# Kernel optimization log

Hardware: AMD Instinct MI355X
Metric: run time of the kernel (lower is better)

The kernel has to match this reference:

```python
import jax, jax.numpy as jnp
import numpy as np

B, S, E = 256, 512, 768          # batch, seq_len, embed_dim (= 2*hidden_dim)
MD = 2 * 384 + 1                 # memory feature dim after location column = 769
HOPS, OUT = 3, 3


def setup_inputs() -> dict:
    key = jax.random.key(0)
    ks = jax.random.split(key, 9)
    memory = jax.random.normal(ks[0], (B, S, E), dtype=jnp.float32)
    aspect = jax.random.normal(ks[1], (B, E), dtype=jnp.float32)
    att_w = jax.random.normal(ks[2], (MD + 2 * E,), dtype=jnp.float32) * 0.02
    att_b = jnp.zeros((1,), dtype=jnp.float32)
    gru_w_ih = jax.random.normal(ks[3], (3 * E, MD), dtype=jnp.float32) * 0.02
    gru_w_hh = jax.random.normal(ks[4], (3 * E, E), dtype=jnp.float32) * 0.02
    gru_b_ih = jnp.zeros((3 * E,), dtype=jnp.float32)
    gru_b_hh = jnp.zeros((3 * E,), dtype=jnp.float32)
    dense_w = jax.random.normal(ks[5], (E, OUT), dtype=jnp.float32) * 0.02
    dense_b = jnp.zeros((OUT,), dtype=jnp.float32)
    memory_len = jax.random.randint(ks[6], (B,), S // 2, S + 1, dtype=jnp.int32)
    left_len = jax.random.randint(ks[7], (B,), 0, 64, dtype=jnp.int32)
    aspect_len = jax.random.randint(ks[8], (B,), 1, 8, dtype=jnp.int32)
    return dict(memory=memory, aspect=aspect, att_w=att_w, att_b=att_b,
                gru_w_ih=gru_w_ih, gru_w_hh=gru_w_hh, gru_b_ih=gru_b_ih,
                gru_b_hh=gru_b_hh, dense_w=dense_w, dense_b=dense_b,
                memory_len=memory_len, left_len=left_len, aspect_len=aspect_len,
                hops=HOPS)


def _locationed_memory(memory, memory_len, left_len, aspect_len):
    # Vectorized form of the nested python loop: per-position location-decay
    # weight and signed-offset column u, only for idx < memory_len.
    dt = memory.dtype
    idx = jnp.arange(memory.shape[1], dtype=jnp.int32)[None, :]   # [1,S]
    start = left_len[:, None]
    alen = aspect_len[:, None]
    mlen = memory_len[:, None]
    before = idx < start
    after_off = idx - start - alen + 1
    u = jnp.where(before, idx - start,
                  jnp.where(idx < start + alen, 0, after_off)).astype(dt)
    l = jnp.where(before, start - idx,
                  jnp.where(idx < start + alen, 0, after_off)).astype(dt)
    valid = idx < mlen
    w = jnp.where(valid, 1.0 - l / mlen.astype(dt), 1.0)
    u = jnp.where(valid, u, 0.0)
    mem = memory * w[:, :, None]
    return jnp.concatenate([mem, u[:, :, None]], axis=-1)        # [B,S,MD]


def _gru_cell(x, h, w_ih, w_hh, b_ih, b_hh):
    gi = x @ w_ih.T + b_ih
    gh = h @ w_hh.T + b_hh
    ir, iz, in_ = jnp.split(gi, 3, axis=-1)
    hr, hz, hn = jnp.split(gh, 3, axis=-1)
    r = jax.nn.sigmoid(ir + hr)
    z = jax.nn.sigmoid(iz + hz)
    n = jnp.tanh(in_ + r * hn)
    return (1.0 - z) * n + z * h


def reference(memory, aspect, att_w, att_b, gru_w_ih, gru_w_hh, gru_b_ih,
              gru_b_hh, dense_w, dense_b, memory_len, left_len, aspect_len,
              hops):
    mem = _locationed_memory(memory, memory_len, left_len, aspect_len)
    # att_linear(cat([mem, et, aspect])) split into three small matvecs
    w_mem = att_w[:MD]
    w_et = att_w[MD:MD + E]
    w_asp = att_w[MD + E:]
    g_static = mem @ w_mem + (aspect @ w_asp)[:, None] + att_b[0]  # [B,S]
    et = jnp.zeros_like(aspect)
    for _ in range(hops):
        g = g_static + (et @ w_et)[:, None]                        # [B,S]
        alpha = jax.nn.softmax(g, axis=1)
        i = jnp.einsum('bs,bsd->bd', alpha, mem)                   # [B,MD]
        et = _gru_cell(i, et, gru_w_ih, gru_w_hh, gru_b_ih, gru_b_hh)
    logits = et @ dense_w + dense_b                                # [B,OUT]
    return logits
```

## Files before the change

kernel.cpp:

```cpp
#include <hip/hip_runtime.h>
#include <math.h>

#define Bn 256
#define Sn 512
#define En 768
#define G3n 2304

typedef __attribute__((ext_vector_type(8))) short short8;
typedef __attribute__((ext_vector_type(4))) float f32x4;

__device__ __forceinline__ float sigmoidf_(float x) { return 1.f / (1.f + __expf(-x)); }
__device__ __forceinline__ float tanhf_(float x) {
  float e = __expf(2.f * x);
  return (e - 1.f) / (e + 1.f);
}

__device__ __forceinline__ unsigned short f2bf(float x) {
  unsigned int u = __builtin_bit_cast(unsigned int, x);
  u += 0x7FFFu + ((u >> 16) & 1u);
  return (unsigned short)(u >> 16);
}
__device__ __forceinline__ float bf2f(unsigned short u) {
  unsigned int x = ((unsigned int)u) << 16;
  return __builtin_bit_cast(float, x);
}

__device__ __forceinline__ void loc_uw(int s, int start, int al, int ml, float& u, float& w) {
  float uu;
  if (s < start)            uu = (float)(s - start);
  else if (s < start + al)  uu = 0.f;
  else                      uu = (float)(s - start - al + 1);
  float l = fabsf(uu);
  if (s < ml) { w = 1.f - l / (float)ml; u = uu; }
  else        { w = 1.f; u = 0.f; }
}

__global__ __launch_bounds__(256) void k_convw(const float* __restrict__ w_ih,
                                               const float* __restrict__ w_hh,
                                               unsigned short* __restrict__ wi_bf,
                                               unsigned short* __restrict__ wh_bf) {
  int t = blockIdx.x * 256 + threadIdx.x;
  int idx = t * 8;
  int r = idx / En, c = idx - r * En;
  const float* src;
  unsigned short* dst;
  if (blockIdx.y == 0) { src = w_ih + (size_t)r * 769 + c; dst = wi_bf + idx; }
  else                 { src = w_hh + (size_t)r * En  + c; dst = wh_bf + idx; }
  unsigned int p[4];
#pragma unroll
  for (int j = 0; j < 4; ++j) {
    unsigned int lo = f2bf(src[2 * j]);
    unsigned int hi = f2bf(src[2 * j + 1]);
    p[j] = lo | (hi << 16);
  }
  *reinterpret_cast<uint4*>(dst) = make_uint4(p[0], p[1], p[2], p[3]);
}

__global__ __launch_bounds__(1024) void k_attn(
    const float* __restrict__ mem, const float* __restrict__ att_w,
    const int* __restrict__ mlen, const int* __restrict__ llen, const int* __restrict__ alen,
    float* __restrict__ pacc, float* __restrict__ pm,
    float* __restrict__ pz, float* __restrict__ piu) {
  __shared__ float accL[16][En];
  __shared__ float mL[16], zL[16], iuL[16];
  int bc = blockIdx.x;
  int b = bc >> 1, half = bc & 1;
  int tid = threadIdx.x, wv = tid >> 6, lane = tid & 63;

  float4 w0 = *reinterpret_cast<const float4*>(att_w + lane * 4);
  float4 w1 = *reinterpret_cast<const float4*>(att_w + 256 + lane * 4);
  float4 w2 = *reinterpret_cast<const float4*>(att_w + 512 + lane * 4);
  float wtail = att_w[En];
  int start = llen[b], al = alen[b], ml = mlen[b];
  int s0row = half * 256 + wv * 16;
  const float* base = mem + ((size_t)b * Sn + s0row) * En;

  float m = -1e30f, z = 0.f, iu = 0.f;
  float4 a0 = {0, 0, 0, 0}, a1 = {0, 0, 0, 0}, a2 = {0, 0, 0, 0};
  float4 v0 = *reinterpret_cast<const float4*>(base + lane * 4);
  float4 v1 = *reinterpret_cast<const float4*>(base + 256 + lane * 4);
  float4 v2 = *reinterpret_cast<const float4*>(base + 512 + lane * 4);

  for (int r = 0; r < 16; ++r) {
    float4 c0 = v0, c1 = v1, c2 = v2;
    if (r < 15) {
      const float* nrow = base + (size_t)(r + 1) * En;
      v0 = *reinterpret_cast<const float4*>(nrow + lane * 4);
      v1 = *reinterpret_cast<const float4*>(nrow + 256 + lane * 4);
      v2 = *reinterpret_cast<const float4*>(nrow + 512 + lane * 4);
    }
    float dot = c0.x * w0.x + c0.y * w0.y + c0.z * w0.z + c0.w * w0.w
              + c1.x * w1.x + c1.y * w1.y + c1.z * w1.z + c1.w * w1.w
              + c2.x * w2.x + c2.y * w2.y + c2.z * w2.z + c2.w * w2.w;
#pragma unroll
    for (int off = 32; off; off >>= 1) dot += __shfl_xor(dot, off);
    int s = s0row + r;
    float u, w;
    loc_uw(s, start, al, ml, u, w);
    float g = w * dot + u * wtail;
    if (g > m) {
      float f = __expf(m - g);
      z *= f; iu *= f;
      a0.x *= f; a0.y *= f; a0.z *= f; a0.w *= f;
      a1.x *= f; a1.y *= f; a1.z *= f; a1.w *= f;
      a2.x *= f; a2.y *= f; a2.z *= f; a2.w *= f;
      m = g;
    }
    float e = __expf(g - m);
    z += e; iu += e * u;
    float sc = e * w;
    a0.x += sc * c0.x; a0.y += sc * c0.y; a0.z += sc * c0.z; a0.w += sc * c0.w;
    a1.x += sc * c1.x; a1.y += sc * c1.y; a1.z += sc * c1.z; a1.w += sc * c1.w;
    a2.x += sc * c2.x; a2.y += sc * c2.y; a2.z += sc * c2.z; a2.w += sc * c2.w;
  }

  *reinterpret_cast<float4*>(&accL[wv][lane * 4])       = a0;
  *reinterpret_cast<float4*>(&accL[wv][256 + lane * 4]) = a1;
  *reinterpret_cast<float4*>(&accL[wv][512 + lane * 4]) = a2;
  if (lane == 0) { mL[wv] = m; zL[wv] = z; iuL[wv] = iu; }
  __syncthreads();

  float M = mL[0];
#pragma unroll
  for (int i = 1; i < 16; ++i) M = fmaxf(M, mL[i]);
  float f[16], Z = 0.f, IU = 0.f;
#pragma unroll
  for (int i = 0; i < 16; ++i) {
    f[i] = __expf(mL[i] - M);
    Z += zL[i] * f[i];
    IU += iuL[i] * f[i];
  }
  if (tid < En) {
    float s = 0.f;
#pragma unroll
    for (int i = 0; i < 16; ++i) s += f[i] * accL[i][tid];
    pacc[(size_t)bc * En + tid] = s;
  }
  if (tid == 0) { pm[bc] = M; pz[bc] = Z; piu[bc] = IU; }
}

__global__ __launch_bounds__(256) void k_comb(
    const float* __restrict__ pacc, const float* __restrict__ pm,
    const float* __restrict__ pz, const float* __restrict__ piu,
    unsigned short* __restrict__ ivec_bf, float* __restrict__ ivtail) {
  int b = blockIdx.x, tid = threadIdx.x;
  float m0 = pm[2 * b], m1 = pm[2 * b + 1];
  float M = fmaxf(m0, m1);
  float f0 = __expf(m0 - M), f1 = __expf(m1 - M);
  float Z = pz[2 * b] * f0 + pz[2 * b + 1] * f1;
  float inv = 1.f / Z;
#pragma unroll
  for (int j = 0; j < 3; ++j) {
    int d = tid + j * 256;
    float s = f0 * pacc[(size_t)(2 * b) * En + d] + f1 * pacc[(size_t)(2 * b + 1) * En + d];
    ivec_bf[(size_t)b * En + d] = f2bf(s * inv);
  }
  if (tid == 0) ivtail[b] = (piu[2 * b] * f0 + piu[2 * b + 1] * f1) * inv;
}

template <int MODE>
__global__ __launch_bounds__(256) void k_fused(
    const unsigned short* __restrict__ Abf, const unsigned short* __restrict__ Wbf,
    const float* __restrict__ ivtail, const float* __restrict__ w_ih,
    const float* __restrict__ b_ih, const float* __restrict__ b_hh,
    float* __restrict__ gi, const unsigned short* __restrict__ et_in_bf,
    unsigned short* __restrict__ et_out_bf) {
  __shared__ unsigned short As[32][72];
  __shared__ unsigned short Bs[3][32][72];
  int e0 = blockIdx.x * 32, m0 = blockIdx.y * 32;
  int tid = threadIdx.x;
  int lane = tid & 63, wv = tid >> 6;
  int wm = wv >> 1, we = wv & 1;
  int l15 = lane & 15, l4 = lane >> 4;

  f32x4 acc[3];
#pragma unroll
  for (int g = 0; g < 3; ++g) { acc[g][0] = 0.f; acc[g][1] = 0.f; acc[g][2] = 0.f; acc[g][3] = 0.f; }

  int arow = tid >> 3, ach = tid & 7;
  for (int k0 = 0; k0 < En; k0 += 64) {
    __syncthreads();
    *reinterpret_cast<uint4*>(&As[arow][ach * 8]) =
        *reinterpret_cast<const uint4*>(Abf + (size_t)(m0 + arow) * En + k0 + ach * 8);
#pragma unroll
    for (int i = 0; i < 3; ++i) {
      int idx = tid + i * 256;
      int row = idx >> 3, ch = idx & 7;
      int g = row >> 5, er = row & 31;
      *reinterpret_cast<uint4*>(&Bs[g][er][ch * 8]) =
          *reinterpret_cast<const uint4*>(Wbf + (size_t)(g * En + e0 + er) * En + k0 + ch * 8);
    }
    __syncthreads();
#pragma unroll
    for (int ks = 0; ks < 2; ++ks) {
      short8 a = *reinterpret_cast<const short8*>(&As[wm * 16 + l15][ks * 32 + l4 * 8]);
#pragma unroll
      for (int g = 0; g < 3; ++g) {
        short8 bfr = *reinterpret_cast<const short8*>(&Bs[g][we * 16 + l15][ks * 32 + l4 * 8]);
        acc[g] = __builtin_amdgcn_mfma_f32_16x16x32_bf16(a, bfr, acc[g], 0, 0, 0);
      }
    }
  }

  int ecol = e0 + we * 16 + l15;
  int mbase = m0 + wm * 16 + l4 * 4;
  float bhr = b_hh[ecol], bhz = b_hh[En + ecol], bhn = b_hh[2 * En + ecol];
  if (MODE == 0) {
    float wn0 = w_ih[(size_t)ecol * 769 + En];
    float wn1 = w_ih[(size_t)(En + ecol) * 769 + En];
    float wn2 = w_ih[(size_t)(2 * En + ecol) * 769 + En];
    float bi0 = b_ih[ecol], bi1 = b_ih[En + ecol], bi2 = b_ih[2 * En + ecol];
#pragma unroll
    for (int j = 0; j < 4; ++j) {
      int m = mbase + j;
      float au = ivtail[m];
      float gr = acc[0][j] + au * wn0 + bi0;
      float gz = acc[1][j] + au * wn1 + bi1;
      float gn = acc[2][j] + au * wn2 + bi2;
      gi[(size_t)m * G3n + ecol]          = gr;
      gi[(size_t)m * G3n + En + ecol]     = gz;
      gi[(size_t)m * G3n + 2 * En + ecol] = gn;
      float r = sigmoidf_(gr + bhr);
      float z = sigmoidf_(gz + bhz);
      float n = tanhf_(gn + r * bhn);
      et_out_bf[(size_t)m * En + ecol] = f2bf((1.f - z) * n);
    }
  } else {
#pragma unroll
    for (int j = 0; j < 4; ++j) {
      int m = mbase + j;
      float rr = sigmoidf_(gi[(size_t)m * G3n + ecol] + acc[0][j] + bhr);
      float zz = sigmoidf_(gi[(size_t)m * G3n + En + ecol] + acc[1][j] + bhz);
      float nn = tanhf_(gi[(size_t)m * G3n + 2 * En + ecol] + rr * (acc[2][j] + bhn));
      float h = bf2f(et_in_bf[(size_t)m * En + ecol]);
      et_out_bf[(size_t)m * En + ecol] = f2bf((1.f - zz) * nn + zz * h);
    }
  }
}

__global__ void k_logits(const unsigned short* __restrict__ et_bf,
                         const float* __restrict__ dw,
                         const float* __restrict__ db, float* __restrict__ out) {
  int gtid = blockIdx.x * blockDim.x + threadIdx.x;
  int wid = gtid >> 6;
  int lane = threadIdx.x & 63;
  if (wid >= Bn) return;
  float s0 = 0.f, s1 = 0.f, s2 = 0.f;
  for (int e = lane; e < En; e += 64) {
    float v = bf2f(et_bf[(size_t)wid * En + e]);
    s0 += v * dw[e * 3 + 0];
    s1 += v * dw[e * 3 + 1];
    s2 += v * dw[e * 3 + 2];
  }
#pragma unroll
  for (int off = 32; off; off >>= 1) {
    s0 += __shfl_xor(s0, off);
    s1 += __shfl_xor(s1, off);
    s2 += __shfl_xor(s2, off);
  }
  if (lane == 0) {
    out[wid * 3 + 0] = s0 + db[0];
    out[wid * 3 + 1] = s1 + db[1];
    out[wid * 3 + 2] = s2 + db[2];
  }
}

extern "C" void kernel_launch(void* const* d_in, const int* in_sizes, int n_in,
                              void* d_out, int out_size, void* d_ws, size_t ws_size,
                              hipStream_t stream) {
  const float* memory   = (const float*)d_in[0];
  const float* att_w    = (const float*)d_in[2];
  const float* gru_w_ih = (const float*)d_in[4];
  const float* gru_w_hh = (const float*)d_in[5];
  const float* gru_b_ih = (const float*)d_in[6];
  const float* gru_b_hh = (const float*)d_in[7];
  const float* dense_w  = (const float*)d_in[8];
  const float* dense_b  = (const float*)d_in[9];
  const int* memory_len = (const int*)d_in[10];
  const int* left_len   = (const int*)d_in[11];
  const int* aspect_len = (const int*)d_in[12];
  float* out = (float*)d_out;

  unsigned short* wi_bf   = (unsigned short*)d_ws;
  unsigned short* wh_bf   = wi_bf + (size_t)G3n * En;
  unsigned short* ivec_bf = wh_bf + (size_t)G3n * En;
  unsigned short* eta_bf  = ivec_bf + (size_t)Bn * En;
  unsigned short* etb_bf  = eta_bf + (size_t)Bn * En;
  unsigned short* etc_bf  = etb_bf + (size_t)Bn * En;
  float* ivtail = (float*)(etc_bf + (size_t)Bn * En);
  float* pm     = ivtail + Bn;
  float* pz     = pm + 2 * Bn;
  float* piu    = pz + 2 * Bn;
  float* pacc   = piu + 2 * Bn;
  float* gi     = pacc + (size_t)2 * Bn * En;

  k_convw<<<dim3(G3n * En / 8 / 256, 2), 256, 0, stream>>>(gru_w_ih, gru_w_hh, wi_bf, wh_bf);
  k_attn<<<dim3(2 * Bn), 1024, 0, stream>>>(memory, att_w, memory_len, left_len, aspect_len,
                                            pacc, pm, pz, piu);
  k_comb<<<dim3(Bn), 256, 0, stream>>>(pacc, pm, pz, piu, ivec_bf, ivtail);
  k_fused<0><<<dim3(En / 32, Bn / 32), 256, 0, stream>>>(
      ivec_bf, wi_bf, ivtail, gru_w_ih, gru_b_ih, gru_b_hh, gi, nullptr, eta_bf);
  k_fused<1><<<dim3(En / 32, Bn / 32), 256, 0, stream>>>(
      eta_bf, wh_bf, nullptr, nullptr, nullptr, gru_b_hh, gi, eta_bf, etb_bf);
  k_fused<1><<<dim3(En / 32, Bn / 32), 256, 0, stream>>>(
      etb_bf, wh_bf, nullptr, nullptr, nullptr, gru_b_hh, gi, etb_bf, etc_bf);
  k_logits<<<dim3(Bn / 4), 256, 0, stream>>>(etc_bf, dense_w, dense_b, out);
}
```

Measured before the change: 126.2 us.

## Merge weight conversion into attention kernel and run GRU hops cooperatively

Result: slower. 202.7 us (+60.6%).

```diff
diff --git a/kernel.cpp b/kernel.cpp
--- a/kernel.cpp
+++ b/kernel.cpp
@@ -1,10 +1,14 @@
 #include <hip/hip_runtime.h>
+#include <hip/hip_cooperative_groups.h>
 #include <math.h>
+
+namespace cg = cooperative_groups;
 
 #define Bn 256
 #define Sn 512
 #define En 768
 #define G3n 2304
+#define COOP_BLOCKS 192
 
 typedef __attribute__((ext_vector_type(8))) short short8;
 typedef __attribute__((ext_vector_type(4))) float f32x4;
@@ -35,37 +39,41 @@
   else        { w = 1.f; u = 0.f; }
 }
 
-__global__ __launch_bounds__(256) void k_convw(const float* __restrict__ w_ih,
-                                               const float* __restrict__ w_hh,
-                                               unsigned short* __restrict__ wi_bf,
-                                               unsigned short* __restrict__ wh_bf) {
-  int t = blockIdx.x * 256 + threadIdx.x;
-  int idx = t * 8;
-  int r = idx / En, c = idx - r * En;
-  const float* src;
-  unsigned short* dst;
-  if (blockIdx.y == 0) { src = w_ih + (size_t)r * 769 + c; dst = wi_bf + idx; }
-  else                 { src = w_hh + (size_t)r * En  + c; dst = wh_bf + idx; }
-  unsigned int p[4];
-#pragma unroll
-  for (int j = 0; j < 4; ++j) {
-    unsigned int lo = f2bf(src[2 * j]);
-    unsigned int hi = f2bf(src[2 * j + 1]);
-    p[j] = lo | (hi << 16);
-  }
-  *reinterpret_cast<uint4*>(dst) = make_uint4(p[0], p[1], p[2], p[3]);
-}
-
-__global__ __launch_bounds__(1024) void k_attn(
+__global__ __launch_bounds__(1024) void k_mega(
     const float* __restrict__ mem, const float* __restrict__ att_w,
     const int* __restrict__ mlen, const int* __restrict__ llen, const int* __restrict__ alen,
+    const float* __restrict__ w_ih, const float* __restrict__ w_hh,
     float* __restrict__ pacc, float* __restrict__ pm,
-    float* __restrict__ pz, float* __restrict__ piu) {
+    float* __restrict__ pz, float* __restrict__ piu,
+    unsigned short* __restrict__ wi_bf, unsigned short* __restrict__ wh_bf) {
   __shared__ float accL[16][En];
   __shared__ float mL[16], zL[16], iuL[16];
   int bc = blockIdx.x;
+  int tid = threadIdx.x;
+
+  if (bc >= 512) {
+    int cb = bc - 512;
+    int mat = cb >= 216;
+    int t = (cb - mat * 216) * 1024 + tid;
+    int idx = t * 8;
+    int r = idx / En, c = idx - r * En;
+    const float* src;
+    unsigned short* dst;
+    if (mat == 0) { src = w_ih + (size_t)r * 769 + c; dst = wi_bf + idx; }
+    else          { src = w_hh + (size_t)r * En  + c; dst = wh_bf + idx; }
+    unsigned int p[4];
+#pragma unroll
+    for (int j = 0; j < 4; ++j) {
+      unsigned int lo = f2bf(src[2 * j]);
+      unsigned int hi = f2bf(src[2 * j + 1]);
+      p[j] = lo | (hi << 16);
+    }
+    *reinterpret_cast<uint4*>(dst) = make_uint4(p[0], p[1], p[2], p[3]);
+    return;
+  }
+
   int b = bc >> 1, half = bc & 1;
-  int tid = threadIdx.x, wv = tid >> 6, lane = tid & 63;
+  int wv = tid >> 6, lane = tid & 63;
 
   float4 w0 = *reinterpret_cast<const float4*>(att_w + lane * 4);
   float4 w1 = *reinterpret_cast<const float4*>(att_w + 256 + lane * 4);
@@ -139,129 +147,140 @@
   if (tid == 0) { pm[bc] = M; pz[bc] = Z; piu[bc] = IU; }
 }
 
-__global__ __launch_bounds__(256) void k_comb(
+__global__ __launch_bounds__(256) void k_coop(
     const float* __restrict__ pacc, const float* __restrict__ pm,
     const float* __restrict__ pz, const float* __restrict__ piu,
-    unsigned short* __restrict__ ivec_bf, float* __restrict__ ivtail) {
-  int b = blockIdx.x, tid = threadIdx.x;
-  float m0 = pm[2 * b], m1 = pm[2 * b + 1];
-  float M = fmaxf(m0, m1);
-  float f0 = __expf(m0 - M), f1 = __expf(m1 - M);
-  float Z = pz[2 * b] * f0 + pz[2 * b + 1] * f1;
-  float inv = 1.f / Z;
-#pragma unroll
-  for (int j = 0; j < 3; ++j) {
-    int d = tid + j * 256;
-    float s = f0 * pacc[(size_t)(2 * b) * En + d] + f1 * pacc[(size_t)(2 * b + 1) * En + d];
-    ivec_bf[(size_t)b * En + d] = f2bf(s * inv);
-  }
-  if (tid == 0) ivtail[b] = (piu[2 * b] * f0 + piu[2 * b + 1] * f1) * inv;
-}
-
-template <int MODE>
-__global__ __launch_bounds__(256) void k_fused(
-    const unsigned short* __restrict__ Abf, const unsigned short* __restrict__ Wbf,
-    const float* __restrict__ ivtail, const float* __restrict__ w_ih,
-    const float* __restrict__ b_ih, const float* __restrict__ b_hh,
-    float* __restrict__ gi, const unsigned short* __restrict__ et_in_bf,
-    unsigned short* __restrict__ et_out_bf) {
+    unsigned short* __restrict__ ivec_bf, float* __restrict__ ivtail,
+    const unsigned short* __restrict__ wi_bf, const unsigned short* __restrict__ wh_bf,
+    const float* __restrict__ w_ih, const float* __restrict__ b_ih,
+    const float* __restrict__ b_hh, float* __restrict__ gi,
+    unsigned short* __restrict__ eta_bf, unsigned short* __restrict__ etb_bf,
+    unsigned short* __restrict__ etc_bf,
+    const float* __restrict__ dw, const float* __restrict__ db,
+    float* __restrict__ out) {
+  cg::grid_group grid = cg::this_grid();
   __shared__ unsigned short As[32][72];
   __shared__ unsigned short Bs[3][32][72];
-  int e0 = blockIdx.x * 32, m0 = blockIdx.y * 32;
-  int tid = threadIdx.x;
-  int lane = tid & 63, wv = tid >> 6;
-  int wm = wv >> 1, we = wv & 1;
+  int bid = blockIdx.x, tid = threadIdx.x;
+
+#pragma unroll
+  for (int it = 0; it < 4; ++it) {
+    int flat = (bid * 256 + tid) + it * (COOP_BLOCKS * 256);
+    int b = flat / En, d = flat - b * En;
+    float m0 = pm[2 * b], m1 = pm[2 * b + 1];
+    float M = fmaxf(m0, m1);
+    float f0 = __expf(m0 - M), f1 = __expf(m1 - M);
+    float inv = 1.f / (pz[2 * b] * f0 + pz[2 * b + 1] * f1);
+    float s = f0 * pacc[(size_t)(2 * b) * En + d] + f1 * pacc[(size_t)(2 * b + 1) * En + d];
+    ivec_bf[flat] = f2bf(s * inv);
+  }
+  if (bid == 0) {
+    int b = tid;
+    float m0 = pm[2 * b], m1 = pm[2 * b + 1];
+    float M = fmaxf(m0, m1);
+    float f0 = __expf(m0 - M), f1 = __expf(m1 - M);
+    float inv = 1.f / (pz[2 * b] * f0 + pz[2 * b + 1] * f1);
+    ivtail[b] = (piu[2 * b] * f0 + piu[2 * b + 1] * f1) * inv;
+  }
+  grid.sync();
+
+  int e0 = (bid % 24) * 32, m0t = (bid / 24) * 32;
+  int lane = tid & 63, wvi = tid >> 6;
+  int wm = wvi >> 1, we = wvi & 1;
   int l15 = lane & 15, l4 = lane >> 4;
-
-  f32x4 acc[3];
-#pragma unroll
-  for (int g = 0; g < 3; ++g) { acc[g][0] = 0.f; acc[g][1] = 0.f; acc[g][2] = 0.f; acc[g][3] = 0.f; }
-
   int arow = tid >> 3, ach = tid & 7;
-  for (int k0 = 0; k0 < En; k0 += 64) {
-    __syncthreads();
-    *reinterpret_cast<uint4*>(&As[arow][ach * 8]) =
-        *reinterpret_cast<const uint4*>(Abf + (size_t)(m0 + arow) * En + k0 + ach * 8);
-#pragma unroll
-    for (int i = 0; i < 3; ++i) {
-      int idx = tid + i * 256;
-      int row = idx >> 3, ch = idx & 7;
-      int g = row >> 5, er = row & 31;
-      *reinterpret_cast<uint4*>(&Bs[g][er][ch * 8]) =
-          *reinterpret_cast<const uint4*>(Wbf + (size_t)(g * En + e0 + er) * En + k0 + ch * 8);
-    }
-    __syncthreads();
-#pragma unroll
-    for (int ks = 0; ks < 2; ++ks) {
-      short8 a = *reinterpret_cast<const short8*>(&As[wm * 16 + l15][ks * 32 + l4 * 8]);
-#pragma unroll
-      for (int g = 0; g < 3; ++g) {
-        short8 bfr = *reinterpret_cast<const short8*>(&Bs[g][we * 16 + l15][ks * 32 + l4 * 8]);
-        acc[g] = __builtin_amdgcn_mfma_f32_16x16x32_bf16(a, bfr, acc[g], 0, 0, 0);
+
+  for (int hop = 0; hop < 3; ++hop) {
+    const unsigned short* Abf = (hop == 0) ? ivec_bf : ((hop == 1) ? eta_bf : etb_bf);
+    const unsigned short* Wbf = (hop == 0) ? wi_bf : wh_bf;
+    unsigned short* Obf = (hop == 0) ? eta_bf : ((hop == 1) ? etb_bf : etc_bf);
+
+    f32x4 acc[3];
+#pragma unroll
+    for (int g = 0; g < 3; ++g) { acc[g][0] = 0.f; acc[g][1] = 0.f; acc[g][2] = 0.f; acc[g][3] = 0.f; }
+
+    for (int k0 = 0; k0 < En; k0 += 64) {
+      __syncthreads();
+      *reinterpret_cast<uint4*>(&As[arow][ach * 8]) =
+          *reinterpret_cast<const uint4*>(Abf + (size_t)(m0t + arow) * En + k0 + ach * 8);
+#pragma unroll
+      for (int i = 0; i < 3; ++i) {
+        int idx = tid + i * 256;
+        int row = idx >> 3, ch = idx & 7;
+        int g = row >> 5, er = row & 31;
+        *reinterpret_cast<uint4*>(&Bs[g][er][ch * 8]) =
+            *reinterpret_cast<const uint4*>(Wbf + (size_t)(g * En + e0 + er) * En + k0 + ch * 8);
       }
-    }
-  }
-
-  int ecol = e0 + we * 16 + l15;
-  int mbase = m0 + wm * 16 + l4 * 4;
-  float bhr = b_hh[ecol], bhz = b_hh[En + ecol], bhn = b_hh[2 * En + ecol];
-  if (MODE == 0) {
-    float wn0 = w_ih[(size_t)ecol * 769 + En];
-    float wn1 = w_ih[(size_t)(En + ecol) * 769 + En];
-    float wn2 = w_ih[(size_t)(2 * En + ecol) * 769 + En];
-    float bi0 = b_ih[ecol], bi1 = b_ih[En + ecol], bi2 = b_ih[2 * En + ecol];
-#pragma unroll
-    for (int j = 0; j < 4; ++j) {
-      int m = mbase + j;
-      float au = ivtail[m];
-      float gr = acc[0][j] + au * wn0 + bi0;
-      float gz = acc[1][j] + au * wn1 + bi1;
-      float gn = acc[2][j] + au * wn2 + bi2;
-      gi[(size_t)m * G3n + ecol]          = gr;
-      gi[(size_t)m * G3n + En + ecol]     = gz;
-      gi[(size_t)m * G3n + 2 * En + ecol] = gn;
-      float r = sigmoidf_(gr + bhr);
-      float z = sigmoidf_(gz + bhz);
-      float n = tanhf_(gn + r * bhn);
-      et_out_bf[(size_t)m * En + ecol] = f2bf((1.f - z) * n);
-    }
-  } else {
-#pragma unroll
-    for (int j = 0; j < 4; ++j) {
-      int m = mbase + j;
-      float rr = sigmoidf_(gi[(size_t)m * G3n + ecol] + acc[0][j] + bhr);
-      float zz = sigmoidf_(gi[(size_t)m * G3n + En + ecol] + acc[1][j] + bhz);
-      float nn = tanhf_(gi[(size_t)m * G3n + 2 * En + ecol] + rr * (acc[2][j] + bhn));
-      float h = bf2f(et_in_bf[(size_t)m * En + ecol]);
-      et_out_bf[(size_t)m * En + ecol] = f2bf((1.f - zz) * nn + zz * h);
-    }
-  }
-}
-
-__global__ void k_logits(const unsigned short* __restrict__ et_bf,
-                         const float* __restrict__ dw,
-                         const float* __restrict__ db, float* __restrict__ out) {
-  int gtid = blockIdx.x * blockDim.x + threadIdx.x;
-  int wid = gtid >> 6;
-  int lane = threadIdx.x & 63;
-  if (wid >= Bn) return;
-  float s0 = 0.f, s1 = 0.f, s2 = 0.f;
-  for (int e = lane; e < En; e += 64) {
-    float v = bf2f(et_bf[(size_t)wid * En + e]);
-    s0 += v * dw[e * 3 + 0];
-    s1 += v * dw[e * 3 + 1];
-    s2 += v * dw[e * 3 + 2];
-  }
-#pragma unroll
-  for (int off = 32; off; off >>= 1) {
-    s0 += __shfl_xor(s0, off);
-    s1 += __shfl_xor(s1, off);
-    s2 += __shfl_xor(s2, off);
-  }
-  if (lane == 0) {
-    out[wid * 3 + 0] = s0 + db[0];
-    out[wid * 3 + 1] = s1 + db[1];
-    out[wid * 3 + 2] = s2 + db[2];
+      __syncthreads();
+#pragma unroll
+      for (int ks = 0; ks < 2; ++ks) {
+        short8 a = *reinterpret_cast<const short8*>(&As[wm * 16 + l15][ks * 32 + l4 * 8]);
+#pragma unroll
+        for (int g = 0; g < 3; ++g) {
+          short8 bfr = *reinterpret_cast<const short8*>(&Bs[g][we * 16 + l15][ks * 32 + l4 * 8]);
+          acc[g] = __builtin_amdgcn_mfma_f32_16x16x32_bf16(a, bfr, acc[g], 0, 0, 0);
+        }
+      }
+    }
+
+    int ecol = e0 + we * 16 + l15;
+    int mbase = m0t + wm * 16 + l4 * 4;
+    float bhr = b_hh[ecol], bhz = b_hh[En + ecol], bhn = b_hh[2 * En + ecol];
+    if (hop == 0) {
+      float wn0 = w_ih[(size_t)ecol * 769 + En];
+      float wn1 = w_ih[(size_t)(En + ecol) * 769 + En];
+      float wn2 = w_ih[(size_t)(2 * En + ecol) * 769 + En];
+      float bi0 = b_ih[ecol], bi1 = b_ih[En + ecol], bi2 = b_ih[2 * En + ecol];
+#pragma unroll
+      for (int j = 0; j < 4; ++j) {
+        int m = mbase + j;
+        float au = ivtail[m];
+        float gr = acc[0][j] + au * wn0 + bi0;
+        float gz = acc[1][j] + au * wn1 + bi1;
+        float gn = acc[2][j] + au * wn2 + bi2;
+        gi[(size_t)m * G3n + ecol]          = gr;
+        gi[(size_t)m * G3n + En + ecol]     = gz;
+        gi[(size_t)m * G3n + 2 * En + ecol] = gn;
+        float r = sigmoidf_(gr + bhr);
+        float z = sigmoidf_(gz + bhz);
+        float n = tanhf_(gn + r * bhn);
+        Obf[(size_t)m * En + ecol] = f2bf((1.f - z) * n);
+      }
+    } else {
+#pragma unroll
+      for (int j = 0; j < 4; ++j) {
+        int m = mbase + j;
+        float rr = sigmoidf_(gi[(size_t)m * G3n + ecol] + acc[0][j] + bhr);
+        float zz = sigmoidf_(gi[(size_t)m * G3n + En + ecol] + acc[1][j] + bhz);
+        float nn = tanhf_(gi[(size_t)m * G3n + 2 * En + ecol] + rr * (acc[2][j] + bhn));
+        float h = bf2f(Abf[(size_t)m * En + ecol]);
+        Obf[(size_t)m * En + ecol] = f2bf((1.f - zz) * nn + zz * h);
+      }
+    }
+    grid.sync();
+  }
+
+  if (bid < 64) {
+    int wv = tid >> 6, lane_ = tid & 63;
+    int row = bid * 4 + wv;
+    float s0 = 0.f, s1 = 0.f, s2 = 0.f;
+    for (int e = lane_; e < En; e += 64) {
+      float v = bf2f(etc_bf[(size_t)row * En + e]);
+      s0 += v * dw[e * 3 + 0];
+      s1 += v * dw[e * 3 + 1];
+      s2 += v * dw[e * 3 + 2];
+    }
+#pragma unroll
+    for (int off = 32; off; off >>= 1) {
+      s0 += __shfl_xor(s0, off);
+      s1 += __shfl_xor(s1, off);
+      s2 += __shfl_xor(s2, off);
+    }
+    if (lane_ == 0) {
+      out[row * 3 + 0] = s0 + db[0];
+      out[row * 3 + 1] = s1 + db[1];
+      out[row * 3 + 2] = s2 + db[2];
+    }
   }
 }
 
@@ -294,15 +313,13 @@
   float* pacc   = piu + 2 * Bn;
   float* gi     = pacc + (size_t)2 * Bn * En;
 
-  k_convw<<<dim3(G3n * En / 8 / 256, 2), 256, 0, stream>>>(gru_w_ih, gru_w_hh, wi_bf, wh_bf);
-  k_attn<<<dim3(2 * Bn), 1024, 0, stream>>>(memory, att_w, memory_len, left_len, aspect_len,
-                                            pacc, pm, pz, piu);
-  k_comb<<<dim3(Bn), 256, 0, stream>>>(pacc, pm, pz, piu, ivec_bf, ivtail);
-  k_fused<0><<<dim3(En / 32, Bn / 32), 256, 0, stream>>>(
-      ivec_bf, wi_bf, ivtail, gru_w_ih, gru_b_ih, gru_b_hh, gi, nullptr, eta_bf);
-  k_fused<1><<<dim3(En / 32, Bn / 32), 256, 0, stream>>>(
-      eta_bf, wh_bf, nullptr, nullptr, nullptr, gru_b_hh, gi, eta_bf, etb_bf);
-  k_fused<1><<<dim3(En / 32, Bn / 32), 256, 0, stream>>>(
-      etb_bf, wh_bf, nullptr, nullptr, nullptr, gru_b_hh, gi, etb_bf, etc_bf);
-  k_logits<<<dim3(Bn / 4), 256, 0, stream>>>(etc_bf, dense_w, dense_b, out);
-}
+  k_mega<<<dim3(944), 1024, 0, stream>>>(memory, att_w, memory_len, left_len, aspect_len,
+                                         gru_w_ih, gru_w_hh, pacc, pm, pz, piu, wi_bf, wh_bf);
+
+  void* args[] = {(void*)&pacc, (void*)&pm, (void*)&pz, (void*)&piu,
+                  (void*)&ivec_bf, (void*)&ivtail, (void*)&wi_bf, (void*)&wh_bf,
+                  (void*)&gru_w_ih, (void*)&gru_b_ih, (void*)&gru_b_hh, (void*)&gi,
+                  (void*)&eta_bf, (void*)&etb_bf, (void*)&etc_bf,
+                  (void*)&dense_w, (void*)&dense_b, (void*)&out};
+  hipLaunchCooperativeKernel((void*)k_coop, dim3(COOP_BLOCKS), dim3(256), args, 0, stream);
+}
```

## Merge weight conversion into attention kernel, fuse logits into last GRU step

Applied to the files above, without the earlier changes.

Result: faster. 120.0 us (-4.9%).

```diff
diff --git a/kernel.cpp b/kernel.cpp
--- a/kernel.cpp
+++ b/kernel.cpp
@@ -35,37 +35,41 @@
   else        { w = 1.f; u = 0.f; }
 }
 
-__global__ __launch_bounds__(256) void k_convw(const float* __restrict__ w_ih,
-                                               const float* __restrict__ w_hh,
-                                               unsigned short* __restrict__ wi_bf,
-                                               unsigned short* __restrict__ wh_bf) {
-  int t = blockIdx.x * 256 + threadIdx.x;
-  int idx = t * 8;
-  int r = idx / En, c = idx - r * En;
-  const float* src;
-  unsigned short* dst;
-  if (blockIdx.y == 0) { src = w_ih + (size_t)r * 769 + c; dst = wi_bf + idx; }
-  else                 { src = w_hh + (size_t)r * En  + c; dst = wh_bf + idx; }
-  unsigned int p[4];
-#pragma unroll
-  for (int j = 0; j < 4; ++j) {
-    unsigned int lo = f2bf(src[2 * j]);
-    unsigned int hi = f2bf(src[2 * j + 1]);
-    p[j] = lo | (hi << 16);
-  }
-  *reinterpret_cast<uint4*>(dst) = make_uint4(p[0], p[1], p[2], p[3]);
-}
-
-__global__ __launch_bounds__(1024) void k_attn(
+__global__ __launch_bounds__(1024) void k_mega(
     const float* __restrict__ mem, const float* __restrict__ att_w,
     const int* __restrict__ mlen, const int* __restrict__ llen, const int* __restrict__ alen,
+    const float* __restrict__ w_ih, const float* __restrict__ w_hh,
     float* __restrict__ pacc, float* __restrict__ pm,
-    float* __restrict__ pz, float* __restrict__ piu) {
+    float* __restrict__ pz, float* __restrict__ piu,
+    unsigned short* __restrict__ wi_bf, unsigned short* __restrict__ wh_bf) {
   __shared__ float accL[16][En];
   __shared__ float mL[16], zL[16], iuL[16];
   int bc = blockIdx.x;
+  int tid = threadIdx.x;
+
+  if (bc >= 512) {
+    int cb = bc - 512;
+    int mat = cb >= 216;
+    int t = (cb - mat * 216) * 1024 + tid;
+    int idx = t * 8;
+    int r = idx / En, c = idx - r * En;
+    const float* src;
+    unsigned short* dst;
+    if (mat == 0) { src = w_ih + (size_t)r * 769 + c; dst = wi_bf + idx; }
+    else          { src = w_hh + (size_t)r * En  + c; dst = wh_bf + idx; }
+    unsigned int p[4];
+#pragma unroll
+    for (int j = 0; j < 4; ++j) {
+      unsigned int lo = f2bf(src[2 * j]);
+      unsigned int hi = f2bf(src[2 * j + 1]);
+      p[j] = lo | (hi << 16);
+    }
+    *reinterpret_cast<uint4*>(dst) = make_uint4(p[0], p[1], p[2], p[3]);
+    return;
+  }
+
   int b = bc >> 1, half = bc & 1;
-  int tid = threadIdx.x, wv = tid >> 6, lane = tid & 63;
+  int wv = tid >> 6, lane = tid & 63;
 
   float4 w0 = *reinterpret_cast<const float4*>(att_w + lane * 4);
   float4 w1 = *reinterpret_cast<const float4*>(att_w + 256 + lane * 4);
@@ -142,8 +146,16 @@
 __global__ __launch_bounds__(256) void k_comb(
     const float* __restrict__ pacc, const float* __restrict__ pm,
     const float* __restrict__ pz, const float* __restrict__ piu,
-    unsigned short* __restrict__ ivec_bf, float* __restrict__ ivtail) {
+    unsigned short* __restrict__ ivec_bf, float* __restrict__ ivtail,
+    const float* __restrict__ db, float* __restrict__ out) {
   int b = blockIdx.x, tid = threadIdx.x;
+  if (b == 0) {
+#pragma unroll
+    for (int j = 0; j < 3; ++j) {
+      int i = tid + j * 256;
+      out[i] = db[i % 3];
+    }
+  }
   float m0 = pm[2 * b], m1 = pm[2 * b + 1];
   float M = fmaxf(m0, m1);
   float f0 = __expf(m0 - M), f1 = __expf(m1 - M);
@@ -163,10 +175,10 @@
     const unsigned short* __restrict__ Abf, const unsigned short* __restrict__ Wbf,
     const float* __restrict__ ivtail, const float* __restrict__ w_ih,
     const float* __restrict__ b_ih, const float* __restrict__ b_hh,
-    float* __restrict__ gi, const unsigned short* __restrict__ et_in_bf,
-    unsigned short* __restrict__ et_out_bf) {
-  __shared__ unsigned short As[32][72];
-  __shared__ unsigned short Bs[3][32][72];
+    float* __restrict__ gi, unsigned short* __restrict__ et_out_bf,
+    const float* __restrict__ dw, float* __restrict__ out) {
+  __shared__ unsigned short As[32][136];
+  __shared__ unsigned short Bs[3][32][136];
   int e0 = blockIdx.x * 32, m0 = blockIdx.y * 32;
   int tid = threadIdx.x;
   int lane = tid & 63, wv = tid >> 6;
@@ -177,22 +189,26 @@
 #pragma unroll
   for (int g = 0; g < 3; ++g) { acc[g][0] = 0.f; acc[g][1] = 0.f; acc[g][2] = 0.f; acc[g][3] = 0.f; }
 
-  int arow = tid >> 3, ach = tid & 7;
-  for (int k0 = 0; k0 < En; k0 += 64) {
+  for (int k0 = 0; k0 < En; k0 += 128) {
     __syncthreads();
-    *reinterpret_cast<uint4*>(&As[arow][ach * 8]) =
-        *reinterpret_cast<const uint4*>(Abf + (size_t)(m0 + arow) * En + k0 + ach * 8);
-#pragma unroll
-    for (int i = 0; i < 3; ++i) {
+#pragma unroll
+    for (int i = 0; i < 2; ++i) {
       int idx = tid + i * 256;
-      int row = idx >> 3, ch = idx & 7;
+      int row = idx >> 4, ch = idx & 15;
+      *reinterpret_cast<uint4*>(&As[row][ch * 8]) =
+          *reinterpret_cast<const uint4*>(Abf + (size_t)(m0 + row) * En + k0 + ch * 8);
+    }
+#pragma unroll
+    for (int i = 0; i < 6; ++i) {
+      int idx = tid + i * 256;
+      int row = idx >> 4, ch = idx & 15;
       int g = row >> 5, er = row & 31;
       *reinterpret_cast<uint4*>(&Bs[g][er][ch * 8]) =
           *reinterpret_cast<const uint4*>(Wbf + (size_t)(g * En + e0 + er) * En + k0 + ch * 8);
     }
     __syncthreads();
 #pragma unroll
-    for (int ks = 0; ks < 2; ++ks) {
+    for (int ks = 0; ks < 4; ++ks) {
       short8 a = *reinterpret_cast<const short8*>(&As[wm * 16 + l15][ks * 32 + l4 * 8]);
 #pragma unroll
       for (int g = 0; g < 3; ++g) {
@@ -205,6 +221,7 @@
   int ecol = e0 + we * 16 + l15;
   int mbase = m0 + wm * 16 + l4 * 4;
   float bhr = b_hh[ecol], bhz = b_hh[En + ecol], bhn = b_hh[2 * En + ecol];
+  float vout[4];
   if (MODE == 0) {
     float wn0 = w_ih[(size_t)ecol * 769 + En];
     float wn1 = w_ih[(size_t)(En + ecol) * 769 + En];
@@ -223,7 +240,7 @@
       float r = sigmoidf_(gr + bhr);
       float z = sigmoidf_(gz + bhz);
       float n = tanhf_(gn + r * bhn);
-      et_out_bf[(size_t)m * En + ecol] = f2bf((1.f - z) * n);
+      vout[j] = (1.f - z) * n;
     }
   } else {
 #pragma unroll
@@ -232,36 +249,40 @@
       float rr = sigmoidf_(gi[(size_t)m * G3n + ecol] + acc[0][j] + bhr);
       float zz = sigmoidf_(gi[(size_t)m * G3n + En + ecol] + acc[1][j] + bhz);
       float nn = tanhf_(gi[(size_t)m * G3n + 2 * En + ecol] + rr * (acc[2][j] + bhn));
-      float h = bf2f(et_in_bf[(size_t)m * En + ecol]);
-      et_out_bf[(size_t)m * En + ecol] = f2bf((1.f - zz) * nn + zz * h);
-    }
-  }
-}
-
-__global__ void k_logits(const unsigned short* __restrict__ et_bf,
-                         const float* __restrict__ dw,
-                         const float* __restrict__ db, float* __restrict__ out) {
-  int gtid = blockIdx.x * blockDim.x + threadIdx.x;
-  int wid = gtid >> 6;
-  int lane = threadIdx.x & 63;
-  if (wid >= Bn) return;
-  float s0 = 0.f, s1 = 0.f, s2 = 0.f;
-  for (int e = lane; e < En; e += 64) {
-    float v = bf2f(et_bf[(size_t)wid * En + e]);
-    s0 += v * dw[e * 3 + 0];
-    s1 += v * dw[e * 3 + 1];
-    s2 += v * dw[e * 3 + 2];
-  }
-#pragma unroll
-  for (int off = 32; off; off >>= 1) {
-    s0 += __shfl_xor(s0, off);
-    s1 += __shfl_xor(s1, off);
-    s2 += __shfl_xor(s2, off);
-  }
-  if (lane == 0) {
-    out[wid * 3 + 0] = s0 + db[0];
-    out[wid * 3 + 1] = s1 + db[1];
-    out[wid * 3 + 2] = s2 + db[2];
+      float h = bf2f(Abf[(size_t)m * En + ecol]);
+      vout[j] = (1.f - zz) * nn + zz * h;
+    }
+  }
+
+  if (MODE != 2) {
+#pragma unroll
+    for (int j = 0; j < 4; ++j)
+      et_out_bf[(size_t)(mbase + j) * En + ecol] = f2bf(vout[j]);
+  } else {
+    float dw0 = dw[ecol * 3 + 0], dw1 = dw[ecol * 3 + 1], dw2 = dw[ecol * 3 + 2];
+    float p[4][3];
+#pragma unroll
+    for (int j = 0; j < 4; ++j) {
+      p[j][0] = vout[j] * dw0;
+      p[j][1] = vout[j] * dw1;
+      p[j][2] = vout[j] * dw2;
+    }
+#pragma unroll
+    for (int off = 1; off < 16; off <<= 1)
+#pragma unroll
+      for (int j = 0; j < 4; ++j) {
+        p[j][0] += __shfl_xor(p[j][0], off);
+        p[j][1] += __shfl_xor(p[j][1], off);
+        p[j][2] += __shfl_xor(p[j][2], off);
+      }
+    if (l15 == 0) {
+#pragma unroll
+      for (int j = 0; j < 4; ++j) {
+        atomicAdd(&out[(mbase + j) * 3 + 0], p[j][0]);
+        atomicAdd(&out[(mbase + j) * 3 + 1], p[j][1]);
+        atomicAdd(&out[(mbase + j) * 3 + 2], p[j][2]);
+      }
+    }
   }
 }
 
@@ -286,23 +307,20 @@
   unsigned short* ivec_bf = wh_bf + (size_t)G3n * En;
   unsigned short* eta_bf  = ivec_bf + (size_t)Bn * En;
   unsigned short* etb_bf  = eta_bf + (size_t)Bn * En;
-  unsigned short* etc_bf  = etb_bf + (size_t)Bn * En;
-  float* ivtail = (float*)(etc_bf + (size_t)Bn * En);
+  float* ivtail = (float*)(etb_bf + (size_t)Bn * En);
   float* pm     = ivtail + Bn;
   float* pz     = pm + 2 * Bn;
   float* piu    = pz + 2 * Bn;
   float* pacc   = piu + 2 * Bn;
   float* gi     = pacc + (size_t)2 * Bn * En;
 
-  k_convw<<<dim3(G3n * En / 8 / 256, 2), 256, 0, stream>>>(gru_w_ih, gru_w_hh, wi_bf, wh_bf);
-  k_attn<<<dim3(2 * Bn), 1024, 0, stream>>>(memory, att_w, memory_len, left_len, aspect_len,
-                                            pacc, pm, pz, piu);
-  k_comb<<<dim3(Bn), 256, 0, stream>>>(pacc, pm, pz, piu, ivec_bf, ivtail);
+  k_mega<<<dim3(944), 1024, 0, stream>>>(memory, att_w, memory_len, left_len, aspect_len,
+                                         gru_w_ih, gru_w_hh, pacc, pm, pz, piu, wi_bf, wh_bf);
+  k_comb<<<dim3(Bn), 256, 0, stream>>>(pacc, pm, pz, piu, ivec_bf, ivtail, dense_b, out);
   k_fused<0><<<dim3(En / 32, Bn / 32), 256, 0, stream>>>(
-      ivec_bf, wi_bf, ivtail, gru_w_ih, gru_b_ih, gru_b_hh, gi, nullptr, eta_bf);
+      ivec_bf, wi_bf, ivtail, gru_w_ih, gru_b_ih, gru_b_hh, gi, eta_bf, nullptr, nullptr);
   k_fused<1><<<dim3(En / 32, Bn / 32), 256, 0, stream>>>(
-      eta_bf, wh_bf, nullptr, nullptr, nullptr, gru_b_hh, gi, eta_bf, etb_bf);
-  k_fused<1><<<dim3(En / 32, Bn / 32), 256, 0, stream>>>(
-      etb_bf, wh_bf, nullptr, nullptr, nullptr, gru_b_hh, gi, etb_bf, etc_bf);
-  k_logits<<<dim3(Bn / 4), 256, 0, stream>>>(etc_bf, dense_w, dense_b, out);
-}
+      eta_bf, wh_bf, nullptr, nullptr, nullptr, gru_b_hh, gi, etb_bf, nullptr, nullptr);
+  k_fused<2><<<dim3(En / 32, Bn / 32), 256, 0, stream>>>(
+      etb_bf, wh_bf, nullptr, nullptr, nullptr, gru_b_hh, gi, nullptr, dense_w, out);
+}
```
